# Performance work log

Hardware: AMD Instinct MI355X
Metric: run time of the kernel (lower is better)

## Reference

```python
import jax, jax.numpy as jnp
from jax import lax
import numpy as np

B, C, T, H, W = 2, 256, 16, 28, 28
RC = C // 16  # reduction channels = 16


def setup_inputs() -> dict:
    key = jax.random.key(0)
    ks = jax.random.split(key, 10)
    s = 0.05
    return {
        "x": jax.random.normal(ks[0], (B, C, T, H, W), jnp.float32),
        "W_down": jax.random.normal(ks[1], (RC, C), jnp.float32) * s,
        "W_down2": jax.random.normal(ks[2], (C, C), jnp.float32) * s,
        "K1": jax.random.normal(ks[3], (RC, 1, 9, 3, 3), jnp.float32) * s,
        "K2": jax.random.normal(ks[4], (RC, 1, 9, 3, 3), jnp.float32) * s,
        "K3": jax.random.normal(ks[5], (RC, 1, 9, 3, 3), jnp.float32) * s,
        "W_back": jax.random.normal(ks[6], (C, RC), jnp.float32) * s,
        "weights": jnp.ones((3,), jnp.float32) / 3.0,
        "weights2": jnp.ones((6,), jnp.float32) / 2.0,
        "weights3": jnp.ones((3,), jnp.float32) / 3.0,
    }


def _dw_conv3d(x, k, pad, dil):
    # depthwise 3D conv: x [B,RC,T,H,W], k [RC,1,9,3,3], groups=RC
    return lax.conv_general_dilated(
        x, k, window_strides=(1, 1, 1),
        padding=[(pad[0], pad[0]), (pad[1], pad[1]), (pad[2], pad[2])],
        rhs_dilation=dil,
        dimension_numbers=("NCDHW", "OIDHW", "NCDHW"),
        feature_group_count=x.shape[1])


def reference(x, W_down, W_down2, K1, K2, K3, W_back, weights, weights2, weights3):
    # weights3 softmax is computed but unused in the original forward; omitted.
    # 1x1x1 conv == channel matmul
    x2 = jnp.einsum("oc,bcthw->bothw", W_down2, x)
    # temporal shift: forward (t+1) and backward (t-1) with edge replication
    x2f = jnp.concatenate([x2[:, :, 1:], x2[:, :, -1:]], axis=2)
    x2b = jnp.concatenate([x2[:, :, :1], x2[:, :, :-1]], axis=2)
    # full spatial-to-spatial affinities per frame: [B,T,H,W,H,W]
    aff1 = jnp.einsum("bcthw,bctsd->bthwsd", x, x2f)
    aff2 = jnp.einsum("bcthw,bctsd->bthwsd", x, x2b)
    cor11 = jnp.einsum("bctsd,bthwsd->bcthw", x2f, jax.nn.sigmoid(aff1) - 0.5)
    cor12 = jnp.einsum("bctsd,bthwsd->bcthw", x2b, jax.nn.sigmoid(aff2) - 0.5)
    features1 = cor11 * weights2[0] + cor12 * weights2[1]
    # reduced-channel gating branch
    xr = jnp.einsum("oc,bcthw->bothw", W_down, x)
    agg = (_dw_conv3d(xr, K1, (4, 1, 1), (1, 1, 1)) * weights[0]
           + _dw_conv3d(xr, K2, (4, 2, 2), (1, 2, 2)) * weights[1]
           + _dw_conv3d(xr, K3, (4, 3, 3), (1, 3, 3)) * weights[2])
    agg = jnp.einsum("oc,bcthw->bothw", W_back, agg)
    return features1 * (jax.nn.sigmoid(agg) - 0.5)
```

## Files before the change

### kernel.cpp

```cpp
#include <hip/hip_runtime.h>
#include <math.h>

#define B_ 2
#define C_ 256
#define T_ 16
#define H_ 28
#define W_ 28
#define HW_ 784
#define RC_ 16
#define QP_ 832
#define CT_STRIDE (T_*HW_)

typedef __attribute__((ext_vector_type(8))) short bf16x8;
typedef __attribute__((ext_vector_type(4))) float f32x4;
typedef __attribute__((ext_vector_type(4))) unsigned short u16x4;

__device__ __forceinline__ f32x4 mfma16(bf16x8 a, bf16x8 b, f32x4 c) {
  return __builtin_amdgcn_mfma_f32_16x16x32_bf16(a, b, c, 0, 0, 0);
}
__device__ __forceinline__ unsigned short f2bf(float f) {
  unsigned u = __float_as_uint(f);
  unsigned r = (u + 0x7FFFu + ((u >> 16) & 1u)) >> 16;
  return (unsigned short)r;
}
__device__ __forceinline__ float bf2f(unsigned short h) {
  return __uint_as_float((unsigned)h << 16);
}
__device__ __forceinline__ void load8(bf16x8* dst, const unsigned short* p) {
  #pragma unroll
  for (int kk = 0; kk < 8; ++kk) dst[kk] = *(const bf16x8*)(p + kk*32);
}
__device__ __forceinline__ void loadV(bf16x8* dst, const unsigned short* v0, int ch) {
  #pragma unroll
  for (int mt = 0; mt < 4; ++mt) {
    dst[mt*2+0] = *(const bf16x8*)(v0 + (size_t)mt*16*T_*QP_ + (size_t)ch*64);
    dst[mt*2+1] = *(const bf16x8*)(v0 + (size_t)mt*16*T_*QP_ + (size_t)ch*64 + 32);
  }
}
__device__ __forceinline__ void frame_swizzle(int id, int& b, int& t, int& p0) {
  const int xcd = id & 7;
  const int j   = id >> 3;
  const int frame = xcd*4 + (j/25);
  const int sub   = j - (j/25)*25;
  b = frame >> 4; t = frame & 15; p0 = sub * 32;
}

__global__ __launch_bounds__(256) void k0_prep(
    const float* __restrict__ W2, const float* __restrict__ Wd,
    unsigned short* __restrict__ x2t_h, unsigned short* __restrict__ x2c_h,
    unsigned short* __restrict__ W2h, unsigned short* __restrict__ W2l,
    unsigned short* __restrict__ Wdh)
{
  int i = blockIdx.x * 256 + threadIdx.x;
  if (i < 2*16*48*256) {
    int bt  = i / (48*256);
    int rem = i - bt*(48*256);
    int q   = 784 + rem / 256;
    int c   = rem & 255;
    x2t_h[((size_t)bt*QP_ + q)*C_ + c] = 0;
    int bct = i / 48;
    int qq  = 784 + (i - bct*48);
    x2c_h[(size_t)bct*QP_ + qq] = 0;
    return;
  }
  int j = i - 2*16*48*256;
  if (j < 65536) {
    float v = W2[j];
    unsigned short h = f2bf(v);
    W2h[j] = h; W2l[j] = f2bf(v - bf2f(h));
    return;
  }
  int k = j - 65536;
  if (k < 4096) Wdh[k] = f2bf(Wd[k]);
}

__global__ __launch_bounds__(256, 2) void k1_mfma(
    const float* __restrict__ x, const unsigned short* __restrict__ W2h,
    const unsigned short* __restrict__ W2l, const unsigned short* __restrict__ Wdh,
    unsigned short* __restrict__ x2t_h, unsigned short* __restrict__ x2c_h,
    float* __restrict__ xr)
{
  __shared__ unsigned short Xth[32][266];
  __shared__ unsigned short Xtl[32][266];
  const int tid  = threadIdx.x;
  const int lane = tid & 63, wv = tid >> 6;
  const int lm = lane & 15, lg = lane >> 4;
  int b, t, p0;
  frame_swizzle(blockIdx.x, b, t, p0);

  {
    const int c = tid;
    const float* xp = x + (((size_t)b*C_ + c)*T_ + t)*HW_ + p0;
    for (int p4 = 0; p4 < 32; p4 += 4) {
      float4 v;
      if (p0 + p4 + 3 < HW_) v = *(const float4*)(xp + p4);
      else { v.x = 0.f; v.y = 0.f; v.z = 0.f; v.w = 0.f; }
      float vv[4] = {v.x, v.y, v.z, v.w};
      #pragma unroll
      for (int jj = 0; jj < 4; ++jj) {
        unsigned short h = f2bf(vv[jj]);
        Xth[p4+jj][c] = h;
        Xtl[p4+jj][c] = f2bf(vv[jj] - bf2f(h));
      }
    }
  }
  __syncthreads();

  bf16x8 xh[2][8], xl[2][8];
  #pragma unroll
  for (int pt = 0; pt < 2; ++pt)
    #pragma unroll
    for (int kk = 0; kk < 8; ++kk) {
      xh[pt][kk] = *(const bf16x8*)&Xth[pt*16 + lm][kk*32 + lg*8];
      xl[pt][kk] = *(const bf16x8*)&Xtl[pt*16 + lm][kk*32 + lg*8];
    }

  const size_t tb = ((size_t)(b*T_ + t)*QP_);
  #pragma unroll
  for (int m = 0; m < 4; ++m) {
    const int o0 = wv*64 + m*16;
    bf16x8 ah[8], al[8];
    load8(ah, W2h + (size_t)(o0 + lm)*C_ + lg*8);
    load8(al, W2l + (size_t)(o0 + lm)*C_ + lg*8);
    f32x4 a0 = {0.f,0.f,0.f,0.f}, a1 = {0.f,0.f,0.f,0.f};
    #pragma unroll
    for (int kk = 0; kk < 8; ++kk) { a0 = mfma16(ah[kk], xh[0][kk], a0); a1 = mfma16(ah[kk], xh[1][kk], a1); }
    #pragma unroll
    for (int kk = 0; kk < 8; ++kk) { a0 = mfma16(al[kk], xh[0][kk], a0); a1 = mfma16(al[kk], xh[1][kk], a1); }
    #pragma unroll
    for (int kk = 0; kk < 8; ++kk) { a0 = mfma16(ah[kk], xl[0][kk], a0); a1 = mfma16(ah[kk], xl[1][kk], a1); }
    #pragma unroll
    for (int pt = 0; pt < 2; ++pt) {
      f32x4 a = pt ? a1 : a0;
      const int p = p0 + pt*16 + lm;
      u16x4 hs;
      #pragma unroll
      for (int r = 0; r < 4; ++r) hs[r] = f2bf(a[r]);
      const size_t rowb = (tb + p)*C_ + o0 + lg*4;
      *(u16x4*)&x2t_h[rowb] = hs;
      #pragma unroll
      for (int r = 0; r < 4; ++r) {
        const int c2 = o0 + lg*4 + r;
        x2c_h[(((size_t)b*C_ + c2)*T_ + t)*QP_ + p] = hs[r];
      }
    }
  }
  if (wv == 0) {
    bf16x8 ad[8];
    load8(ad, Wdh + (size_t)lm*C_ + lg*8);
    f32x4 r0 = {0.f,0.f,0.f,0.f}, r1 = {0.f,0.f,0.f,0.f};
    #pragma unroll
    for (int kk = 0; kk < 8; ++kk) { r0 = mfma16(ad[kk], xh[0][kk], r0); r1 = mfma16(ad[kk], xh[1][kk], r1); }
    #pragma unroll
    for (int kk = 0; kk < 8; ++kk) { r0 = mfma16(ad[kk], xl[0][kk], r0); r1 = mfma16(ad[kk], xl[1][kk], r1); }
    #pragma unroll
    for (int pt = 0; pt < 2; ++pt) {
      const int p = p0 + pt*16 + lm;
      if (p < HW_) {
        f32x4 rr = pt ? r1 : r0;
        #pragma unroll
        for (int r = 0; r < 4; ++r)
          xr[((size_t)(b*RC_ + lg*4 + r)*T_ + t)*HW_ + p] = rr[r];
      }
    }
  }
}

__global__ __launch_bounds__(256) void k2_dwconv(
    const float* __restrict__ xr, const float* __restrict__ K1w,
    const float* __restrict__ K2w, const float* __restrict__ K3w,
    const float* __restrict__ wts, float* __restrict__ agg)
{
  __shared__ float slab[9][HW_];
  __shared__ float kw[3][81];
  const int tid = threadIdx.x;
  const int t  = blockIdx.x;
  const int br = blockIdx.y;
  const int r = br & 15;
  const size_t chbase = (size_t)br * T_ * HW_;
  for (int idx = tid; idx < 9*HW_; idx += 256) {
    int kd = idx / HW_, pp = idx - kd*HW_;
    int tt = t + kd - 4;
    slab[kd][pp] = (tt >= 0 && tt < T_) ? xr[chbase + (size_t)tt*HW_ + pp] : 0.f;
  }
  for (int idx = tid; idx < 3*81; idx += 256) {
    int kk = idx / 81, rem = idx - kk*81;
    const float* Ksrc = (kk == 0) ? K1w : ((kk == 1) ? K2w : K3w);
    kw[kk][rem] = Ksrc[r*81 + rem];
  }
  __syncthreads();
  const float w0 = wts[0], w1 = wts[1], w2v = wts[2];
  for (int p = tid; p < HW_; p += 256) {
    int h = p / W_, w = p - h*W_;
    float s0 = 0.f, s1 = 0.f, s2 = 0.f;
    for (int kd = 0; kd < 9; ++kd) {
      #pragma unroll
      for (int kh = 0; kh < 3; ++kh) {
        #pragma unroll
        for (int kwi = 0; kwi < 3; ++kwi) {
          const int widx = kd*9 + kh*3 + kwi;
          { int hh = h + (kh-1), ww = w + (kwi-1);
            if (hh >= 0 && hh < H_ && ww >= 0 && ww < W_)
              s0 += kw[0][widx] * slab[kd][hh*W_ + ww]; }
          { int hh = h + (kh-1)*2, ww = w + (kwi-1)*2;
            if (hh >= 0 && hh < H_ && ww >= 0 && ww < W_)
              s1 += kw[1][widx] * slab[kd][hh*W_ + ww]; }
          { int hh = h + (kh-1)*3, ww = w + (kwi-1)*3;
            if (hh >= 0 && hh < H_ && ww >= 0 && ww < W_)
              s2 += kw[2][widx] * slab[kd][hh*W_ + ww]; }
        }
      }
    }
    agg[chbase + (size_t)t*HW_ + p] = w0*s0 + w1*s1 + w2v*s2;
  }
}

#define CHUNK2(KH, KHN, CH, PB, PF)                                            \
{                                                                              \
  bf16x8 vv[8];                                                                \
  loadV(vv, vchunk0, (CH));                    \
  if (PF) load8(KHN, khp0 + (size_t)((CH)+1)*64*C_);      \
  f32x4 S0 = {0.f,0.f,0.f,0.f}, S1 = {0.f,0.f,0.f,0.f};                        \
  _Pragma("unroll")                                                            \
  for (int kk = 0; kk < 8; ++kk) {                          \
    S0 = mfma16(qh[0][kk], KH[kk], S0);                                        \
    S1 = mfma16(qh[1][kk], KH[kk], S1);                                        \
  }                                                                            \
  _Pragma("unroll")                                                            \
  for (int kk = 0; kk < 8; ++kk) {                    \
    bf16x8 ql0 = *(const bf16x8*)&Ql[lm][kk*32 + lg*8];                        \
    bf16x8 ql1 = *(const bf16x8*)&Ql[16 + lm][kk*32 + lg*8];                   \
    S0 = mfma16(ql0, KH[kk], S0);                                              \
    S1 = mfma16(ql1, KH[kk], S1);                                              \
  }                                                                            \
  _Pragma("unroll")                                                            \
  for (int r = 0; r < 4; ++r) {                         \
    float pa = wdir * (1.f/(1.f+__expf(-S0[r])) - 0.5f);                       \
    float pb = wdir * (1.f/(1.f+__expf(-S1[r])) - 0.5f);                       \
    Pls[PB][lg*4+r][wv*16+lm]    = f2bf(pa);                                   \
    Pls[PB][16+lg*4+r][wv*16+lm] = f2bf(pb);                                   \
  }                                                                            \
  __builtin_amdgcn_sched_barrier(0);                                           \
  asm volatile("s_waitcnt lgkmcnt(0)" ::: "memory");                           \
  __builtin_amdgcn_s_barrier();                                                \
  __builtin_amdgcn_sched_barrier(0);                                           \
  {                                                                            \
    bf16x8 pbf[2][2];                                                          \
    _Pragma("unroll")                                                          \
    for (int nt = 0; nt < 2; ++nt)                                             \
      _Pragma("unroll")                                                        \
      for (int ks = 0; ks < 2; ++ks)                                           \
        pbf[nt][ks] = *(const bf16x8*)&Pls[PB][nt*16+lm][ks*32+lg*8];          \
    _Pragma("unroll")                                                          \
    for (int mt = 0; mt < 4; ++mt) {                                           \
      _Pragma("unroll")                                                        \
      for (int ks = 0; ks < 2; ++ks) {                                         \
        O[mt][0] = mfma16(vv[mt*2+ks], pbf[0][ks], O[mt][0]);                  \
        O[mt][1] = mfma16(vv[mt*2+ks], pbf[1][ks], O[mt][1]);                  \
      }                                                                        \
    }                                                                          \
  }                                                                            \
}

__global__ __launch_bounds__(256, 2) void k3_attn_mfma(
    const float* __restrict__ x, const unsigned short* __restrict__ x2t_h,
    const unsigned short* __restrict__ x2c_h,
    const float* __restrict__ w2arr, float* __restrict__ outF)
{
  __shared__ unsigned short Qh[32][266];
  __shared__ unsigned short Ql[32][266];
  __shared__ unsigned short Pls[2][32][74];
  const int tid  = threadIdx.x;
  const int lane = tid & 63, wv = tid >> 6;
  const int lm = lane & 15, lg = lane >> 4;
  int b, t, p0;
  frame_swizzle(blockIdx.x, b, t, p0);

  {
    const int c = tid;
    const float* xp = x + (((size_t)b*C_ + c)*T_ + t)*HW_ + p0;
    for (int p4 = 0; p4 < 32; p4 += 4) {
      float4 v;
      if (p0 + p4 + 3 < HW_) v = *(const float4*)(xp + p4);
      else { v.x = 0.f; v.y = 0.f; v.z = 0.f; v.w = 0.f; }
      float vvv[4] = {v.x, v.y, v.z, v.w};
      #pragma unroll
      for (int jj = 0; jj < 4; ++jj) {
        unsigned short h = f2bf(vvv[jj]);
        Qh[p4+jj][c] = h;
        Ql[p4+jj][c] = f2bf(vvv[jj] - bf2f(h));
      }
    }
  }
  __syncthreads();

  bf16x8 qh[2][8];
  #pragma unroll
  for (int pt = 0; pt < 2; ++pt)
    #pragma unroll
    for (int kk = 0; kk < 8; ++kk)
      qh[pt][kk] = *(const bf16x8*)&Qh[pt*16 + lm][kk*32 + lg*8];

  f32x4 O[4][2];
  #pragma unroll
  for (int mt = 0; mt < 4; ++mt)
    #pragma unroll
    for (int nt = 0; nt < 2; ++nt)
      O[mt][nt] = (f32x4){0.f, 0.f, 0.f, 0.f};

  const float wd0 = w2arr[0], wd1 = w2arr[1];

  for (int dir = 0; dir < 2; ++dir) {
    const int ts = (dir == 0) ? (t < T_-1 ? t+1 : T_-1) : (t > 0 ? t-1 : 0);
    const float wdir = (dir == 0) ? wd0 : wd1;
    const size_t kf = ((size_t)b*T_ + ts)*QP_;
    const unsigned short* khp0 = x2t_h + (kf + wv*16 + lm)*C_ + lg*8;
    const unsigned short* vchunk0 =
        x2c_h + (((size_t)b*C_ + wv*64 + lm)*T_ + ts)*QP_ + lg*8;

    bf16x8 khA[8], khB[8];
    load8(khA, khp0);
    for (int cc = 0; cc < 6; ++cc) {
      CHUNK2(khA, khB, (cc*2),   0, 1)
      CHUNK2(khB, khA, (cc*2+1), 1, 1)
    }
    CHUNK2(khA, khB, 12, 0, 0)
    __syncthreads();
  }
  #pragma unroll
  for (int mt = 0; mt < 4; ++mt) {
    const int cbase = wv*64 + mt*16 + lg*4;
    #pragma unroll
    for (int nt = 0; nt < 2; ++nt) {
      const int p = p0 + nt*16 + lm;
      if (p < HW_) {
        #pragma unroll
        for (int r = 0; r < 4; ++r)
          outF[(((size_t)b*C_ + (cbase + r))*T_ + t)*HW_ + p] = O[mt][nt][r];
      }
    }
  }
}

#define K4_PT 112
__global__ __launch_bounds__(256) void k4_gate(
    const float* __restrict__ agg, const float* __restrict__ Wb,
    float* __restrict__ out)
{
  __shared__ float aggl[RC_][K4_PT];
  const int tid = threadIdx.x;
  const int bt  = blockIdx.y;
  const int b = bt >> 4, t = bt & 15;
  const int p0 = blockIdx.x * K4_PT;
  for (int idx = tid; idx < RC_*K4_PT; idx += 256) {
    int r = idx / K4_PT, p = idx - r*K4_PT;
    aggl[r][p] = agg[((size_t)(b*RC_ + r)*T_ + t)*HW_ + p0 + p];
  }
  __syncthreads();
  const int o = tid;
  float wb[RC_];
  #pragma unroll
  for (int r4 = 0; r4 < RC_; r4 += 4) {
    float4 v = *(const float4*)(Wb + o*RC_ + r4);
    wb[r4] = v.x; wb[r4+1] = v.y; wb[r4+2] = v.z; wb[r4+3] = v.w;
  }
  float* orow = out + ((size_t)(b*C_ + o)*T_ + t)*HW_ + p0;
  for (int p = 0; p < K4_PT; ++p) {
    float g = 0.f;
    #pragma unroll
    for (int r = 0; r < RC_; ++r) g += wb[r] * aggl[r][p];
    float sig = 1.f / (1.f + __expf(-g));
    orow[p] *= (sig - 0.5f);
  }
}

extern "C" void kernel_launch(void* const* d_in, const int* in_sizes, int n_in,
                              void* d_out, int out_size, void* d_ws, size_t ws_size,
                              hipStream_t stream)
{
  const float* x     = (const float*)d_in[0];
  const float* Wd    = (const float*)d_in[1];
  const float* W2    = (const float*)d_in[2];
  const float* K1w   = (const float*)d_in[3];
  const float* K2w   = (const float*)d_in[4];
  const float* K3w   = (const float*)d_in[5];
  const float* Wb    = (const float*)d_in[6];
  const float* wts   = (const float*)d_in[7];
  const float* w2arr = (const float*)d_in[8];

  const size_t NX2T = (size_t)B_ * T_ * QP_ * C_;
  unsigned short* x2t_h = (unsigned short*)d_ws;
  unsigned short* x2c_h = x2t_h + NX2T;
  float* xr  = (float*)(x2c_h + NX2T);
  float* agg = xr + (size_t)B_*RC_*T_*HW_;
  unsigned short* W2h = (unsigned short*)(agg + (size_t)B_*RC_*T_*HW_);
  unsigned short* W2l = W2h + 65536;
  unsigned short* Wdh = W2l + 65536;
  float* out = (float*)d_out;

  k0_prep <<<1808, 256, 0, stream>>>(W2, Wd, x2t_h, x2c_h, W2h, W2l, Wdh);
  k1_mfma <<<dim3(800), 256, 0, stream>>>(x, W2h, W2l, Wdh, x2t_h, x2c_h, xr);
  k2_dwconv<<<dim3(T_, B_*RC_), 256, 0, stream>>>(xr, K1w, K2w, K3w, wts, agg);
  k3_attn_mfma<<<dim3(800), 256, 0, stream>>>(x, x2t_h, x2c_h, w2arr, out);
  k4_gate <<<dim3(HW_/K4_PT, B_*T_), 256, 0, stream>>>(agg, Wb, out);
}
```

Measured before the change: 409.4 us.

## Double attention query tile to 64 and drop split-bf16 low-part query correction

After: 393.4 us. 3.9% less time.

```diff
diff --git a/kernel.cpp b/kernel.cpp
--- a/kernel.cpp
+++ b/kernel.cpp
@@ -43,6 +43,13 @@
   const int frame = xcd*4 + (j/25);
   const int sub   = j - (j/25)*25;
   b = frame >> 4; t = frame & 15; p0 = sub * 32;
+}
+__device__ __forceinline__ void frame_swizzle64(int id, int& b, int& t, int& p0) {
+  const int xcd = id & 7;
+  const int j   = id >> 3;
+  const int frame = xcd*4 + (j/13);
+  const int sub   = j - (j/13)*13;
+  b = frame >> 4; t = frame & 15; p0 = sub * 64;
 }
 
 __global__ __launch_bounds__(256) void k0_prep(
@@ -215,48 +222,46 @@
   }
 }
 
-#define CHUNK2(KH, KHN, CH, PB, PF)                                            \
+#define CHUNK64(KH, KHN, CH, PB, PF)                                           \
 {                                                                              \
   bf16x8 vv[8];                                                                \
   loadV(vv, vchunk0, (CH));                    \
   if (PF) load8(KHN, khp0 + (size_t)((CH)+1)*64*C_);      \
   f32x4 S0 = {0.f,0.f,0.f,0.f}, S1 = {0.f,0.f,0.f,0.f};                        \
+  f32x4 S2 = {0.f,0.f,0.f,0.f}, S3 = {0.f,0.f,0.f,0.f};                        \
   _Pragma("unroll")                                                            \
-  for (int kk = 0; kk < 8; ++kk) {                          \
+  for (int kk = 0; kk < 8; ++kk) {               \
     S0 = mfma16(qh[0][kk], KH[kk], S0);                                        \
     S1 = mfma16(qh[1][kk], KH[kk], S1);                                        \
-  }                                                                            \
-  _Pragma("unroll")                                                            \
-  for (int kk = 0; kk < 8; ++kk) {                    \
-    bf16x8 ql0 = *(const bf16x8*)&Ql[lm][kk*32 + lg*8];                        \
-    bf16x8 ql1 = *(const bf16x8*)&Ql[16 + lm][kk*32 + lg*8];                   \
-    S0 = mfma16(ql0, KH[kk], S0);                                              \
-    S1 = mfma16(ql1, KH[kk], S1);                                              \
+    bf16x8 q2 = *(const bf16x8*)&Qh[32 + lm][kk*32 + lg*8];                    \
+    bf16x8 q3 = *(const bf16x8*)&Qh[48 + lm][kk*32 + lg*8];                    \
+    S2 = mfma16(q2, KH[kk], S2);                      \
+    S3 = mfma16(q3, KH[kk], S3);                                               \
   }                                                                            \
   _Pragma("unroll")                                                            \
   for (int r = 0; r < 4; ++r) {                         \
     float pa = wdir * (1.f/(1.f+__expf(-S0[r])) - 0.5f);                       \
     float pb = wdir * (1.f/(1.f+__expf(-S1[r])) - 0.5f);                       \
+    float pc = wdir * (1.f/(1.f+__expf(-S2[r])) - 0.5f);                       \
+    float pd = wdir * (1.f/(1.f+__expf(-S3[r])) - 0.5f);                       \
     Pls[PB][lg*4+r][wv*16+lm]    = f2bf(pa);                                   \
     Pls[PB][16+lg*4+r][wv*16+lm] = f2bf(pb);                                   \
+    Pls[PB][32+lg*4+r][wv*16+lm] = f2bf(pc);                                   \
+    Pls[PB][48+lg*4+r][wv*16+lm] = f2bf(pd);                                   \
   }                                                                            \
   __builtin_amdgcn_sched_barrier(0);                                           \
   asm volatile("s_waitcnt lgkmcnt(0)" ::: "memory");                           \
   __builtin_amdgcn_s_barrier();                                                \
   __builtin_amdgcn_sched_barrier(0);                                           \
   {                                                                            \
-    bf16x8 pbf[2][2];                                                          \
     _Pragma("unroll")                                                          \
-    for (int nt = 0; nt < 2; ++nt)                                             \
+    for (int nt = 0; nt < 4; ++nt) {                                           \
+      bf16x8 pb0 = *(const bf16x8*)&Pls[PB][nt*16+lm][lg*8];                   \
+      bf16x8 pb1 = *(const bf16x8*)&Pls[PB][nt*16+lm][32+lg*8];                \
       _Pragma("unroll")                                                        \
-      for (int ks = 0; ks < 2; ++ks)                                           \
-        pbf[nt][ks] = *(const bf16x8*)&Pls[PB][nt*16+lm][ks*32+lg*8];          \
-    _Pragma("unroll")                                                          \
-    for (int mt = 0; mt < 4; ++mt) {                                           \
-      _Pragma("unroll")                                                        \
-      for (int ks = 0; ks < 2; ++ks) {                                         \
-        O[mt][0] = mfma16(vv[mt*2+ks], pbf[0][ks], O[mt][0]);                  \
-        O[mt][1] = mfma16(vv[mt*2+ks], pbf[1][ks], O[mt][1]);                  \
+      for (int mt = 0; mt < 4; ++mt) {                                         \
+        O[mt][nt] = mfma16(vv[mt*2+0], pb0, O[mt][nt]);                        \
+        O[mt][nt] = mfma16(vv[mt*2+1], pb1, O[mt][nt]);                        \
       }                                                                        \
     }                                                                          \
   }                                                                            \
@@ -267,29 +272,24 @@
     const unsigned short* __restrict__ x2c_h,
     const float* __restrict__ w2arr, float* __restrict__ outF)
 {
-  __shared__ unsigned short Qh[32][266];
-  __shared__ unsigned short Ql[32][266];
-  __shared__ unsigned short Pls[2][32][74];
+  __shared__ unsigned short Qh[64][266];
+  __shared__ unsigned short Pls[2][64][74];
   const int tid  = threadIdx.x;
   const int lane = tid & 63, wv = tid >> 6;
   const int lm = lane & 15, lg = lane >> 4;
   int b, t, p0;
-  frame_swizzle(blockIdx.x, b, t, p0);
+  frame_swizzle64(blockIdx.x, b, t, p0);
 
   {
     const int c = tid;
     const float* xp = x + (((size_t)b*C_ + c)*T_ + t)*HW_ + p0;
-    for (int p4 = 0; p4 < 32; p4 += 4) {
+    for (int p4 = 0; p4 < 64; p4 += 4) {
       float4 v;
       if (p0 + p4 + 3 < HW_) v = *(const float4*)(xp + p4);
       else { v.x = 0.f; v.y = 0.f; v.z = 0.f; v.w = 0.f; }
       float vvv[4] = {v.x, v.y, v.z, v.w};
       #pragma unroll
-      for (int jj = 0; jj < 4; ++jj) {
-        unsigned short h = f2bf(vvv[jj]);
-        Qh[p4+jj][c] = h;
-        Ql[p4+jj][c] = f2bf(vvv[jj] - bf2f(h));
-      }
+      for (int jj = 0; jj < 4; ++jj) Qh[p4+jj][c] = f2bf(vvv[jj]);
     }
   }
   __syncthreads();
@@ -301,11 +301,11 @@
     for (int kk = 0; kk < 8; ++kk)
       qh[pt][kk] = *(const bf16x8*)&Qh[pt*16 + lm][kk*32 + lg*8];
 
-  f32x4 O[4][2];
+  f32x4 O[4][4];
   #pragma unroll
   for (int mt = 0; mt < 4; ++mt)
     #pragma unroll
-    for (int nt = 0; nt < 2; ++nt)
+    for (int nt = 0; nt < 4; ++nt)
       O[mt][nt] = (f32x4){0.f, 0.f, 0.f, 0.f};
 
   const float wd0 = w2arr[0], wd1 = w2arr[1];
@@ -321,17 +321,17 @@
     bf16x8 khA[8], khB[8];
     load8(khA, khp0);
     for (int cc = 0; cc < 6; ++cc) {
-      CHUNK2(khA, khB, (cc*2),   0, 1)
-      CHUNK2(khB, khA, (cc*2+1), 1, 1)
-    }
-    CHUNK2(khA, khB, 12, 0, 0)
+      CHUNK64(khA, khB, (cc*2),   0, 1)
+      CHUNK64(khB, khA, (cc*2+1), 1, 1)
+    }
+    CHUNK64(khA, khB, 12, 0, 0)
     __syncthreads();
   }
   #pragma unroll
   for (int mt = 0; mt < 4; ++mt) {
     const int cbase = wv*64 + mt*16 + lg*4;
     #pragma unroll
-    for (int nt = 0; nt < 2; ++nt) {
+    for (int nt = 0; nt < 4; ++nt) {
       const int p = p0 + nt*16 + lm;
       if (p < HW_) {
         #pragma unroll
@@ -401,6 +401,6 @@
   k0_prep <<<1808, 256, 0, stream>>>(W2, Wd, x2t_h, x2c_h, W2h, W2l, Wdh);
   k1_mfma <<<dim3(800), 256, 0, stream>>>(x, W2h, W2l, Wdh, x2t_h, x2c_h, xr);
   k2_dwconv<<<dim3(T_, B_*RC_), 256, 0, stream>>>(xr, K1w, K2w, K3w, wts, agg);
-  k3_attn_mfma<<<dim3(800), 256, 0, stream>>>(x, x2t_h, x2c_h, w2arr, out);
+  k3_attn_mfma<<<dim3(416), 256, 0, stream>>>(x, x2t_h, x2c_h, w2arr, out);
   k4_gate <<<dim3(HW_/K4_PT, B_*T_), 256, 0, stream>>>(agg, Wb, out);
 }
```
